# Kernel tuning notes

Measured on AMD Instinct MI355X. Metric: run time of the kernel, lower is better.

## Reference

```python
import jax, jax.numpy as jnp
import numpy as np
from jax import lax

NUM_HEADS = 16
PADDING_L = 15


def setup_inputs() -> dict:
    key = jax.random.key(0)
    k1, k2 = jax.random.split(key)
    T, B, C = 2048, 8, 1024
    H, K = NUM_HEADS, 31
    x = jax.random.normal(k1, (T, B, C), dtype=jnp.float32)
    weight = jax.random.normal(k2, (H, 1, K), dtype=jnp.float32)
    bias = jnp.zeros((C,), dtype=jnp.float32)
    return {"x": x, "weight": weight, "bias": bias}


def reference(x, weight, bias):
    # x: (T, B, C); weight: (H, 1, K); bias: (C,)
    T, B, C = x.shape
    H, _, K = weight.shape
    R = C // H  # channels per head sharing one kernel
    # weight_softmax=True: normalize kernel taps per head
    w = jax.nn.softmax(weight.reshape(H, K), axis=-1)
    # Expand the shared per-head kernel to one kernel per channel (depthwise conv)
    w_full = jnp.repeat(w, R, axis=0).reshape(C, 1, K)  # (C, 1, K) = OIH
    xb = jnp.transpose(x, (1, 2, 0))  # (B, C, T) = NCH
    # Depthwise correlation: y[t] = sum_k w[k] * x[t + k - padding_l]
    y = lax.conv_general_dilated(
        xb, w_full,
        window_strides=(1,),
        padding=[(PADDING_L, K - 1 - PADDING_L)],
        feature_group_count=C,
        dimension_numbers=("NCH", "OIH", "NCH"),
    )  # (B, C, T)
    out = jnp.transpose(y, (2, 0, 1))  # back to (T, B, C)
    return out + bias.reshape(1, 1, -1)
```

## Files before the change

kernel.cpp:

```cpp
#include <hip/hip_runtime.h>
#include <utility>
#include <cmath>

constexpr int T = 2048;
constexpr int B = 8;
constexpr int C = 1024;
constexpr int H = 16;
constexpr int K = 31;
constexpr int PAD = 15;
constexpr int NBC = B * C;
constexpr int BC_TILE = 64;
constexpr int T_TILE = 64;
constexpr int ROWS = T_TILE + K - 1;
constexpr int BLOCK = 256;
constexpr int WAVES = BLOCK / 64;
constexpr int TT = T_TILE / WAVES;
constexpr int WIN = TT + K - 1;

__device__ __forceinline__ float uniform_f(float v) {
    return __int_as_float(__builtin_amdgcn_readfirstlane(__float_as_int(v)));
}

__device__ __forceinline__ void gld_lds_b32(const float* gsrc, float* ldst) {
    __builtin_amdgcn_global_load_lds(
        (const __attribute__((address_space(1))) unsigned int*)gsrc,
        (__attribute__((address_space(3))) unsigned int*)ldst,
        4, 0, 0);
}

template <int KK>
__device__ __forceinline__ void tap(float (&acc)[TT], const float (&xv)[WIN], float wk) {
#pragma unroll
    for (int i = 0; i < TT; ++i)
        acc[i] = fmaf(wk, xv[i + KK], acc[i]);
}

template <int... Ks>
__device__ __forceinline__ void all_taps(float (&acc)[TT], const float (&xv)[WIN],
                                         const float (&w)[K],
                                         std::integer_sequence<int, Ks...>) {
    (tap<Ks>(acc, xv, w[Ks]), ...);
}

__global__ __launch_bounds__(BLOCK, 6) void lconv_tbc_kernel(
    const float* __restrict__ x,
    const float* __restrict__ wgt,
    const float* __restrict__ bias,
    float* __restrict__ out)
{
    __shared__ float xs[ROWS * BC_TILE];
    __shared__ float sw[K];

    const int tid  = threadIdx.x;
    const int wave = tid >> 6;
    const int lane = tid & 63;
    const int bc0  = blockIdx.x * BC_TILE;
    const int t0   = blockIdx.y * T_TILE;
    const int tstart = t0 - PAD;

    for (int r = wave; r < ROWS; r += WAVES) {
        const int tg = tstart + r;
        if (tg >= 0 && tg < T) {
            gld_lds_b32(x + (size_t)tg * NBC + bc0 + lane, &xs[r * BC_TILE]);
        } else {
            xs[r * BC_TILE + lane] = 0.0f;
        }
    }

    if (wave == 0) {
        const int head = (bc0 & (C - 1)) >> 6;
        float raw = (lane < K) ? wgt[head * K + lane] : -INFINITY;
        float m = raw;
        #pragma unroll
        for (int off = 32; off >= 1; off >>= 1) m = fmaxf(m, __shfl_xor(m, off));
        float e = (lane < K) ? expf(raw - m) : 0.0f;
        float s = e;
        #pragma unroll
        for (int off = 32; off >= 1; off >>= 1) s += __shfl_xor(s, off);
        if (lane < K) sw[lane] = e / s;
    }

    __syncthreads();

    float w[K];
    #pragma unroll
    for (int k = 0; k < K; ++k) w[k] = uniform_f(sw[k]);

    float xv[WIN];
    const float* xrow = &xs[(wave * TT) * BC_TILE + lane];
    #pragma unroll
    for (int j = 0; j < WIN; ++j)
        xv[j] = xrow[j * BC_TILE];

    float acc[TT];
    #pragma unroll
    for (int i = 0; i < TT; ++i) acc[i] = 0.0f;

    all_taps(acc, xv, w, std::make_integer_sequence<int, K>{});

    const int c = (bc0 + lane) & (C - 1);
    const float bb = bias[c];
    float* op = out + (size_t)(t0 + wave * TT) * NBC + bc0 + lane;
    #pragma unroll
    for (int i = 0; i < TT; ++i)
        op[(size_t)i * NBC] = acc[i] + bb;
}

extern "C" void kernel_launch(void* const* d_in, const int* in_sizes, int n_in,
                              void* d_out, int out_size, void* d_ws, size_t ws_size,
                              hipStream_t stream) {
    const float* x    = (const float*)d_in[0];
    const float* wgt  = (const float*)d_in[1];
    const float* bias = (const float*)d_in[2];
    float* out        = (float*)d_out;

    dim3 grid(NBC / BC_TILE, T / T_TILE);
    lconv_tbc_kernel<<<grid, dim3(BLOCK), 0, stream>>>(x, wgt, bias, out);
}
```

Baseline: 37.97 us.

## Double-buffer LDS tiles across four time tiles per block with 128-bit async loads

Each block now processes four consecutive time tiles, staging the next tile into a second LDS buffer while computing the current one, with manual vmcnt waits and barriers. Global-to-LDS loads become 16-byte per lane, and out-of-range rows read from a zeroed workspace buffer instead of being written with conditional stores. The goal is to hide load latency and cut per-block setup such as the softmax. In exchange the grid has four times fewer blocks, launch bounds drop to 1, a memset is added to every launch, and the hard-coded vmcnt literal is fragile.

```diff
diff --git a/kernel.cpp b/kernel.cpp
--- a/kernel.cpp
+++ b/kernel.cpp
@@ -12,20 +12,25 @@
 constexpr int BC_TILE = 64;
 constexpr int T_TILE = 64;
 constexpr int ROWS = T_TILE + K - 1;
+constexpr int ROWS4 = 96;
 constexpr int BLOCK = 256;
 constexpr int WAVES = BLOCK / 64;
 constexpr int TT = T_TILE / WAVES;
 constexpr int WIN = TT + K - 1;
+constexpr int TPB = 4;
+constexpr int NCHUNK = (T / T_TILE) / TPB;
+constexpr int GPW = ROWS4 / 4 / WAVES;
+static_assert(GPW == 6, "vmcnt literal below assumes 6");
 
 __device__ __forceinline__ float uniform_f(float v) {
     return __int_as_float(__builtin_amdgcn_readfirstlane(__float_as_int(v)));
 }
 
-__device__ __forceinline__ void gld_lds_b32(const float* gsrc, float* ldst) {
+__device__ __forceinline__ void gld_lds_b128(const float* gsrc, float* ldst) {
     __builtin_amdgcn_global_load_lds(
         (const __attribute__((address_space(1))) unsigned int*)gsrc,
         (__attribute__((address_space(3))) unsigned int*)ldst,
-        4, 0, 0);
+        16, 0, 0);
 }
 
 template <int KK>
@@ -42,30 +47,42 @@
     (tap<Ks>(acc, xv, w[Ks]), ...);
 }
 
-__global__ __launch_bounds__(BLOCK, 6) void lconv_tbc_kernel(
+__global__ __launch_bounds__(BLOCK, 1) void lconv_tbc_kernel(
     const float* __restrict__ x,
     const float* __restrict__ wgt,
     const float* __restrict__ bias,
+    const float* __restrict__ zbuf,
     float* __restrict__ out)
 {
-    __shared__ float xs[ROWS * BC_TILE];
+    __shared__ float xs[2][ROWS4 * BC_TILE];
     __shared__ float sw[K];
 
     const int tid  = threadIdx.x;
     const int wave = tid >> 6;
     const int lane = tid & 63;
     const int bc0  = blockIdx.x * BC_TILE;
-    const int t0   = blockIdx.y * T_TILE;
-    const int tstart = t0 - PAD;
+    const int tchunk0 = blockIdx.y * (TPB * T_TILE);
 
-    for (int r = wave; r < ROWS; r += WAVES) {
-        const int tg = tstart + r;
-        if (tg >= 0 && tg < T) {
-            gld_lds_b32(x + (size_t)tg * NBC + bc0 + lane, &xs[r * BC_TILE]);
-        } else {
-            xs[r * BC_TILE + lane] = 0.0f;
+    const int lane_row = lane >> 4;
+    const int lane_col = (lane & 15) * 4;
+    const ptrdiff_t lane_off = (ptrdiff_t)lane_row * NBC + lane_col;
+    const float* zsrc = zbuf + lane_col;
+
+    auto stage_tile = [&](int buf, int ttile) {
+        const int tst = ttile - PAD;
+        float* ldsb = &xs[buf][(wave * GPW) * 4 * BC_TILE];
+        #pragma unroll
+        for (int s = 0; s < GPW; ++s) {
+            const int g   = wave * GPW + s;
+            const int tg0 = tst + 4 * g;
+            const int tg  = tg0 + lane_row;
+            const float* src = x + (ptrdiff_t)tg0 * NBC + bc0 + lane_off;
+            const float* p   = ((unsigned)tg < (unsigned)T) ? src : zsrc;
+            gld_lds_b128(p, ldsb + s * 4 * BC_TILE);
         }
-    }
+    };
+
+    stage_tile(0, tchunk0);
 
     if (wave == 0) {
         const int head = (bc0 & (C - 1)) >> 6;
@@ -85,25 +102,38 @@
     float w[K];
     #pragma unroll
     for (int k = 0; k < K; ++k) w[k] = uniform_f(sw[k]);
+    const float bb = bias[(bc0 + lane) & (C - 1)];
 
-    float xv[WIN];
-    const float* xrow = &xs[(wave * TT) * BC_TILE + lane];
-    #pragma unroll
-    for (int j = 0; j < WIN; ++j)
-        xv[j] = xrow[j * BC_TILE];
+    #pragma unroll 1
+    for (int it = 0; it < TPB; ++it) {
+        const int cur = it & 1;
+        if (it + 1 < TPB) {
+            stage_tile(cur ^ 1, tchunk0 + (it + 1) * T_TILE);
+            asm volatile("s_waitcnt vmcnt(6)" ::: "memory");
+        } else {
+            asm volatile("s_waitcnt vmcnt(0)" ::: "memory");
+        }
+        __builtin_amdgcn_s_barrier();
 
-    float acc[TT];
-    #pragma unroll
-    for (int i = 0; i < TT; ++i) acc[i] = 0.0f;
+        float xv[WIN];
+        const float* xrow = &xs[cur][(wave * TT) * BC_TILE + lane];
+        #pragma unroll
+        for (int j = 0; j < WIN; ++j)
+            xv[j] = xrow[j * BC_TILE];
 
-    all_taps(acc, xv, w, std::make_integer_sequence<int, K>{});
+        float acc[TT];
+        #pragma unroll
+        for (int i = 0; i < TT; ++i) acc[i] = 0.0f;
 
-    const int c = (bc0 + lane) & (C - 1);
-    const float bb = bias[c];
-    float* op = out + (size_t)(t0 + wave * TT) * NBC + bc0 + lane;
-    #pragma unroll
-    for (int i = 0; i < TT; ++i)
-        op[(size_t)i * NBC] = acc[i] + bb;
+        all_taps(acc, xv, w, std::make_integer_sequence<int, K>{});
+
+        float* op = out + (size_t)(tchunk0 + it * T_TILE + wave * TT) * NBC + bc0 + lane;
+        #pragma unroll
+        for (int i = 0; i < TT; ++i)
+            op[(size_t)i * NBC] = acc[i] + bb;
+
+        __builtin_amdgcn_s_barrier();
+    }
 }
 
 extern "C" void kernel_launch(void* const* d_in, const int* in_sizes, int n_in,
@@ -113,7 +143,10 @@
     const float* wgt  = (const float*)d_in[1];
     const float* bias = (const float*)d_in[2];
     float* out        = (float*)d_out;
+    float* zbuf       = (float*)d_ws;
 
-    dim3 grid(NBC / BC_TILE, T / T_TILE);
-    lconv_tbc_kernel<<<grid, dim3(BLOCK), 0, stream>>>(x, wgt, bias, out);
+    hipMemsetAsync(zbuf, 0, 256, stream);
+
+    dim3 grid(NBC / BC_TILE, NCHUNK);
+    lconv_tbc_kernel<<<grid, dim3(BLOCK), 0, stream>>>(x, wgt, bias, zbuf, out);
 }
```

Result: slower. 39.62 us (+4.3%).
